# Optimization experiments

Hardware: AMD Instinct MI355X
Metric: run time of the kernel (lower is better)

## Reference

```python
import jax, jax.numpy as jnp
import numpy as np

B = 1
T_FRAMES = 512
LDIM = 512
D = 512
H = 8
DH = 64
L = 8
FF = 2048
CTX = 250
RATIOS = (8, 6, 5, 4)
MAX_PERIOD = 10000.0


def setup_inputs() -> dict:
    key = jax.random.key(0)
    ks = iter(jax.random.split(key, 80))
    def rn(shape, s=0.02):
        return jax.random.normal(next(ks), shape, jnp.float32) * s
    inp = {}
    inp['latent'] = rn((B, LDIM, T_FRAMES), 1.0)
    inp['emb_std'] = jax.random.uniform(next(ks), (LDIM,), jnp.float32, 0.5, 1.5)
    inp['emb_mean'] = rn((LDIM,), 0.1)
    inp['quant_w'] = rn((D, LDIM)); inp['quant_b'] = jnp.zeros((D,))
    inp['up_w'] = rn((D, D, 4)); inp['up_b'] = jnp.zeros((D,))
    inp['n1w'] = jnp.ones((L, D)); inp['n1b'] = jnp.zeros((L, D))
    inp['ipw'] = rn((L, 3 * D, D)); inp['ipb'] = jnp.zeros((L, 3 * D))
    inp['opw'] = rn((L, D, D)); inp['opb'] = jnp.zeros((L, D))
    inp['ls1'] = jnp.full((L, D), 0.01)
    inp['n2w'] = jnp.ones((L, D)); inp['n2b'] = jnp.zeros((L, D))
    inp['l1w'] = rn((L, FF, D)); inp['l1b'] = jnp.zeros((L, FF))
    inp['l2w'] = rn((L, D, FF)); inp['l2b'] = jnp.zeros((L, D))
    inp['ls2'] = jnp.full((L, D), 0.01)
    inp['tproj_w'] = rn((D, D)); inp['tproj_b'] = jnp.zeros((D,))
    inp['dc0_w'] = rn((1024, D, 7)); inp['dc0_b'] = jnp.zeros((1024,))
    ch = 1024
    for i, r in enumerate(RATIOS, 1):
        co = ch // 2
        inp['t%d_w' % i] = rn((ch, co, 2 * r)); inp['t%d_b' % i] = jnp.zeros((co,))
        inp['r%da_w' % i] = rn((co // 2, co, 3)); inp['r%da_b' % i] = jnp.zeros((co // 2,))
        inp['r%db_w' % i] = rn((co, co // 2, 1)); inp['r%db_b' % i] = jnp.zeros((co,))
        ch = co
    inp['df_w'] = rn((1, 64, 7)); inp['df_b'] = jnp.zeros((1,))
    return {k: jnp.asarray(v, jnp.float32) for k, v in inp.items()}


def _ln(x, w, b):
    m = x.mean(-1, keepdims=True)
    v = ((x - m) ** 2).mean(-1, keepdims=True)
    return (x - m) / jnp.sqrt(v + 1e-5) * w + b


def _rope(x, cos, sin):
    # x: (B,T,H,DH); cos/sin: (T,1,DH//2)
    b_, t_, h_, d_ = x.shape
    xr = x.reshape(b_, t_, h_, d_ // 2, 2)
    re, im = xr[..., 0], xr[..., 1]
    out = jnp.stack([re * cos - im * sin, re * sin + im * cos], axis=-1)
    return out.reshape(b_, t_, h_, d_)


def _conv(x, w, b, stride=1):
    # StreamingConv1d non-streaming: left-pad by k-stride (zeros), then valid conv.
    k = w.shape[-1]
    pad = k - stride
    if pad > 0:
        x = jnp.pad(x, ((0, 0), (0, 0), (pad, 0)))
    y = jax.lax.conv_general_dilated(x, w, (stride,), 'VALID',
                                     dimension_numbers=('NCH', 'OIH', 'NCH'))
    return y + b[None, :, None]


def _convtr(x, w, b, stride):
    # torch ConvTranspose1d, padding=0: w is (in, out, k); L_out=(L-1)*stride+k
    k = w.shape[-1]
    w2 = jnp.swapaxes(jnp.flip(w, -1), 0, 1)  # (out, in, k)
    y = jax.lax.conv_general_dilated(x, w2, (1,), [(k - 1, k - 1)],
                                     lhs_dilation=(stride,),
                                     dimension_numbers=('NCH', 'OIH', 'NCH'))
    return y + b[None, :, None]


def _forward(latent, emb_std, emb_mean, quant_w, quant_b, up_w, up_b,
             n1w, n1b, ipw, ipb, opw, opb, ls1, n2w, n2b, l1w, l1b, l2w, l2b, ls2,
             tproj_w, tproj_b, dc0_w, dc0_b,
             t1_w, t1_b, r1a_w, r1a_b, r1b_w, r1b_b,
             t2_w, t2_b, r2a_w, r2a_b, r2b_w, r2b_b,
             t3_w, t3_b, r3a_w, r3a_b, r3b_w, r3b_b,
             t4_w, t4_b, r4a_w, r4a_b, r4b_w, r4b_b,
             df_w, df_b):
    # denormalize + quantizer output proj (1x1 conv)
    x = latent * emb_std[None, :, None] + emb_mean[None, :, None]
    x = jnp.einsum('od,bdt->bot', quant_w, x) + quant_b[None, :, None]
    # upsample (raw convtr, no trimming)
    x = _convtr(x, up_w, up_b, 2)
    z = jnp.swapaxes(x, 1, 2)  # (B, T, D)
    T = z.shape[1]
    # windowed causal additive mask: attend to previous `CTX` positions incl. self
    pos = jnp.arange(T)
    delta = pos[:, None] - pos[None, :]
    mask = jnp.where((delta >= 0) & (delta < CTX), 0.0, -jnp.inf).astype(jnp.float32)
    # RoPE tables (offset = 0)
    fr = jnp.exp(jnp.arange(DH // 2, dtype=jnp.float32) * (-np.log(MAX_PERIOD) * 2.0 / DH))
    ang = jnp.arange(T, dtype=jnp.float32)[:, None, None] * fr  # (T,1,DH//2)
    cos, sin = jnp.cos(ang), jnp.sin(ang)
    scale = 1.0 / np.sqrt(DH)

    def step(h, p):
        n1w_, n1b_, ipw_, ipb_, opw_, opb_, ls1_, n2w_, n2b_, l1w_, l1b_, l2w_, l2b_, ls2_ = p
        hn = _ln(h, n1w_, n1b_)
        qkv = (jnp.einsum('btd,ed->bte', hn, ipw_) + ipb_).reshape(B, T, 3, H, DH)
        q, k, v = qkv[:, :, 0], qkv[:, :, 1], qkv[:, :, 2]
        q = _rope(q, cos, sin)
        k = _rope(k, cos, sin)
        s = jnp.einsum('bqhd,bkhd->bhqk', q, k) * scale + mask
        a = jax.nn.softmax(s, axis=-1)
        o = jnp.einsum('bhqk,bkhd->bqhd', a, v).reshape(B, T, D)
        o = jnp.einsum('btd,ed->bte', o, opw_) + opb_
        h = h + ls1_ * o
        hn2 = _ln(h, n2w_, n2b_)
        ff = jax.nn.gelu(jnp.einsum('btd,fd->btf', hn2, l1w_) + l1b_, approximate=False)
        ff = jnp.einsum('btf,df->btd', ff, l2w_) + l2b_
        h = h + ls2_ * ff
        return h, None

    z, _ = jax.lax.scan(step, z, (n1w, n1b, ipw, ipb, opw, opb, ls1,
                                  n2w, n2b, l1w, l1b, l2w, l2b, ls2))
    z = jnp.einsum('btd,ed->bte', z, tproj_w) + tproj_b
    z = jnp.swapaxes(z, 1, 2)  # (B, D, T)
    # SEANet decoder
    z = _conv(z, dc0_w, dc0_b, 1)
    stages = ((t1_w, t1_b, r1a_w, r1a_b, r1b_w, r1b_b, 8),
              (t2_w, t2_b, r2a_w, r2a_b, r2b_w, r2b_b, 6),
              (t3_w, t3_b, r3a_w, r3a_b, r3b_w, r3b_b, 5),
              (t4_w, t4_b, r4a_w, r4a_b, r4b_w, r4b_b, 4))
    for tw, tb, raw_, rab_, rbw_, rbb_, st in stages:
        z = jax.nn.elu(z)
        z = _convtr(z, tw, tb, st)
        v2 = _conv(jax.nn.elu(z), raw_, rab_, 1)
        v2 = _conv(jax.nn.elu(v2), rbw_, rbb_, 1)
        z = z + v2  # residual block skip
    z = jax.nn.elu(z)
    z = _conv(z, df_w, df_b, 1)
    return z  # (B, 1, T_samples)


def reference(latent, emb_std, emb_mean, quant_w, quant_b, up_w, up_b,
              n1w, n1b, ipw, ipb, opw, opb, ls1, n2w, n2b, l1w, l1b, l2w, l2b, ls2,
              tproj_w, tproj_b, dc0_w, dc0_b,
              t1_w, t1_b, r1a_w, r1a_b, r1b_w, r1b_b,
              t2_w, t2_b, r2a_w, r2a_b, r2b_w, r2b_b,
              t3_w, t3_b, r3a_w, r3a_b, r3b_w, r3b_b,
              t4_w, t4_b, r4a_w, r4a_b, r4b_w, r4b_b,
              df_w, df_b):
    return _forward(latent, emb_std, emb_mean, quant_w, quant_b, up_w, up_b,
                    n1w, n1b, ipw, ipb, opw, opb, ls1, n2w, n2b, l1w, l1b, l2w, l2b, ls2,
                    tproj_w, tproj_b, dc0_w, dc0_b,
                    t1_w, t1_b, r1a_w, r1a_b, r1b_w, r1b_b,
                    t2_w, t2_b, r2a_w, r2a_b, r2b_w, r2b_b,
                    t3_w, t3_b, r3a_w, r3a_b, r3b_w, r3b_b,
                    t4_w, t4_b, r4a_w, r4a_b, r4b_w, r4b_b,
                    df_w, df_b)
```

## Files before the change

kernel.cpp:

```cpp
#include <hip/hip_runtime.h>
#include <math.h>

typedef __attribute__((ext_vector_type(8))) short short8;
typedef __attribute__((ext_vector_type(4))) float f32x4;

#define MFMA16(a, b, c) __builtin_amdgcn_mfma_f32_16x16x32_bf16((a), (b), (c), 0, 0, 0)

__device__ __forceinline__ unsigned bfu(float f) {
    unsigned u = __float_as_uint(f);
    return (u + 0x7fffu + ((u >> 16) & 1u)) >> 16;
}

__device__ __forceinline__ void swz_block(unsigned& bx, unsigned& by, unsigned& bz) {
    unsigned gx = gridDim.x, gy = gridDim.y, gz = gridDim.z;
    unsigned nb = gx * gy * gz;
    unsigned d = blockIdx.x + gx * (blockIdx.y + gy * blockIdx.z);
    if ((nb & 7u) == 0u) d = (d & 7u) * (nb >> 3) + (d >> 3);
    bx = d % gx;
    unsigned r = d / gx;
    by = r % gy;
    bz = r / gy;
}

static constexpr int TT   = 1026;
static constexpr int T_S1 = 8216;
static constexpr int T_S2 = 49302;
static constexpr int T_S3 = 246515;
static constexpr int T_S4 = 986064;

static constexpr int NCH    = 8;
static constexpr int LC     = T_S4 / NCH;
static constexpr int LE_MAX = LC + 8;

static constexpr size_t O_X0  = 0;
static constexpr size_t O_XQ  = 262144;
static constexpr size_t O_XU  = 524288;
static constexpr size_t O_Z   = 1049600;
static constexpr size_t O_HN  = 1574912;
static constexpr size_t O_QKV = 2100224;
static constexpr size_t O_AO  = 3676160;
static constexpr size_t O_FF  = 4201472;
static constexpr size_t O_COS = 6302720;
static constexpr size_t O_SIN = 6335552;
static constexpr size_t O_ZT  = 6368384;
static constexpr size_t O_ZC  = 6893696;
static constexpr size_t O_D0  = 7419008;
static constexpr size_t O_Z1  = 8469632;
static constexpr size_t O_V1  = 12676224;
static constexpr size_t O_PS1 = 16000000;
static constexpr size_t O_Z2  = 31553920;
static constexpr size_t O_V2  = 0;
static constexpr size_t O_Z3  = 0;
static constexpr size_t O_V3  = 31553920;
static constexpr size_t O_Z4C = 31553920;
static constexpr size_t O_VAC = 39442944;

static inline int cdiv(int a, int b) { return (a + b - 1) / b; }

__global__ __launch_bounds__(256) void addp_k(float* __restrict__ y,
    const float* __restrict__ p, unsigned long long pstr, int np, int n4)
{
    int i = blockIdx.x * 256 + threadIdx.x;
    if (i >= n4) return;
    float4 s = ((float4*)y)[i];
    for (int z = 0; z < np; z++) {
        float4 q = ((const float4*)(p + (size_t)z * pstr))[i];
        s.x += q.x; s.y += q.y; s.z += q.z; s.w += q.w;
    }
    ((float4*)y)[i] = s;
}

__global__ __launch_bounds__(256) void embed_k(const float* __restrict__ lat,
    const float* __restrict__ sd, const float* __restrict__ mn, float* __restrict__ y)
{
    int i = blockIdx.x * 256 + threadIdx.x;
    if (i >= 512 * 512) return;
    int c = i >> 9;
    y[i] = lat[i] * sd[c] + mn[c];
}

__global__ __launch_bounds__(256) void rope_tables(float* __restrict__ cs, float* __restrict__ sn)
{
    int idx = blockIdx.x * 256 + threadIdx.x;
    if (idx >= TT * 32) return;
    int i = idx & 31;
    int t = idx >> 5;
    float fr = expf(-(float)i * (logf(10000.f) / 32.f));
    float ang = (float)t * fr;
    cs[idx] = cosf(ang);
    sn[idx] = sinf(ang);
}

__global__ __launch_bounds__(256) void rope_apply(float* __restrict__ qkv,
    const float* __restrict__ cs, const float* __restrict__ sn)
{
    int idx = blockIdx.x * 256 + threadIdx.x;
    if (idx >= TT * 8 * 32) return;
    int i = idx & 31;
    int h = (idx >> 5) & 7;
    int t = idx >> 8;
    float c = cs[t * 32 + i], s = sn[t * 32 + i];
    size_t base = (size_t)t * 1536 + h * 64 + 2 * i;
    float re = qkv[base], im = qkv[base + 1];
    qkv[base]     = re * c - im * s;
    qkv[base + 1] = re * s + im * c;
    base += 512;
    re = qkv[base]; im = qkv[base + 1];
    qkv[base]     = re * c - im * s;
    qkv[base + 1] = re * s + im * c;
}

__global__ __launch_bounds__(256) void transpose_k(const float* __restrict__ in,
    float* __restrict__ out, int R, int C)
{
    __shared__ float tile[32][33];
    int c0 = blockIdx.x * 32, r0 = blockIdx.y * 32;
    int tx = threadIdx.x & 31, ty = threadIdx.x >> 5;
    for (int dy = ty; dy < 32; dy += 8) {
        int r = r0 + dy, c = c0 + tx;
        tile[dy][tx] = (r < R && c < C) ? in[(size_t)r * C + c] : 0.f;
    }
    __syncthreads();
    for (int dy = ty; dy < 32; dy += 8) {
        int c = c0 + dy, r = r0 + tx;
        if (c < C && r < R) out[(size_t)c * R + r] = tile[tx][dy];
    }
}

__global__ __launch_bounds__(256) void ln_kernel(const float* __restrict__ x,
    const float* __restrict__ w, const float* __restrict__ b, float* __restrict__ y)
{
    int t = blockIdx.x, tid = threadIdx.x;
    const float* xr = x + (size_t)t * 512;
    float v0 = xr[tid], v1 = xr[tid + 256];
    float s = v0 + v1, q = v0 * v0 + v1 * v1;
    for (int off = 32; off; off >>= 1) {
        s += __shfl_down(s, off);
        q += __shfl_down(q, off);
    }
    __shared__ float ss[4], qq[4], mb[2];
    int wid = tid >> 6, lane = tid & 63;
    if (lane == 0) { ss[wid] = s; qq[wid] = q; }
    __syncthreads();
    if (tid == 0) {
        float S = ss[0] + ss[1] + ss[2] + ss[3];
        float Q = qq[0] + qq[1] + qq[2] + qq[3];
        float m = S * (1.f / 512.f);
        float var = Q * (1.f / 512.f) - m * m;
        mb[0] = m;
        mb[1] = rsqrtf(var + 1e-5f);
    }
    __syncthreads();
    float m = mb[0], inv = mb[1];
    y[(size_t)t * 512 + tid]       = (v0 - m) * inv * w[tid] + b[tid];
    y[(size_t)t * 512 + tid + 256] = (v1 - m) * inv * w[tid + 256] + b[tid + 256];
}

__global__ __launch_bounds__(256) void attn_kernel(const float* __restrict__ qkv,
    float* __restrict__ o)
{
    int t = blockIdx.x, h = blockIdx.y, tid = threadIdx.x;
    __shared__ float sq[64];
    __shared__ float sp[256];
    __shared__ float red[256];
    __shared__ float pacc[4][64];
    int klo = t - 249; if (klo < 0) klo = 0;
    int kc = t - klo + 1;
    if (tid < 64) sq[tid] = qkv[(size_t)t * 1536 + h * 64 + tid];
    __syncthreads();
    float sval = -3.0e38f;
    if (tid < kc) {
        const float* kr = qkv + (size_t)(klo + tid) * 1536 + 512 + h * 64;
        float d = 0.f;
#pragma unroll 8
        for (int i = 0; i < 64; i++) d += sq[i] * kr[i];
        sval = d * 0.125f;
    }
    red[tid] = sval;
    __syncthreads();
    for (int s2 = 128; s2 > 0; s2 >>= 1) {
        if (tid < s2) red[tid] = fmaxf(red[tid], red[tid + s2]);
        __syncthreads();
    }
    float m = red[0];
    __syncthreads();
    float p = (tid < kc) ? __expf(sval - m) : 0.f;
    sp[tid] = p;
    red[tid] = p;
    __syncthreads();
    for (int s2 = 128; s2 > 0; s2 >>= 1) {
        if (tid < s2) red[tid] += red[tid + s2];
        __syncthreads();
    }
    float inv = 1.f / red[0];
    int d = tid & 63, g = tid >> 6;
    float a = 0.f;
#pragma unroll 4
    for (int kk = g; kk < kc; kk += 4)
        a += sp[kk] * qkv[(size_t)(klo + kk) * 1536 + 1024 + h * 64 + d];
    pacc[g][d] = a;
    __syncthreads();
    if (tid < 64) {
        float r = (pacc[0][tid] + pacc[1][tid] + pacc[2][tid] + pacc[3][tid]) * inv;
        o[(size_t)t * 512 + h * 64 + tid] = r;
    }
}

template <int EPI>
__global__ __launch_bounds__(256, 3) void mfma_gemm(const float* __restrict__ A,
    const float* __restrict__ Wt, const float* __restrict__ bias,
    const float* __restrict__ ls, float* __restrict__ C, int M, int N, int K)
{
    constexpr int STR = 72;
    __shared__ unsigned short sA[128 * STR];
    __shared__ unsigned short sB[128 * STR];
    int tid = threadIdx.x;
    unsigned bxs, bys, bzs; swz_block(bxs, bys, bzs);
    int m0 = bys * 128, n0 = bxs * 128;
    int w = tid >> 6, lane = tid & 63;
    int wm = (w >> 1) * 64, wn = (w & 1) * 64;
    int row15 = lane & 15, q8 = (lane >> 4) * 8;
    int rb = tid >> 3;
    int sg = (tid & 7) * 8;
    f32x4 acc[4][4] = {};
    float4 av[8], bv[8];
    const float4 z4 = make_float4(0.f, 0.f, 0.f, 0.f);

    auto prefetch = [&](int k0) {
#pragma unroll
        for (int it = 0; it < 4; it++) {
            int r = rb + it * 32;
            int gm = m0 + r;
            if (gm < M) {
                const float4* p = (const float4*)(A + (size_t)gm * K + k0 + sg);
                av[2 * it] = p[0]; av[2 * it + 1] = p[1];
            } else { av[2 * it] = z4; av[2 * it + 1] = z4; }
            int gn = n0 + r;
            if (gn < N) {
                const float4* p = (const float4*)(Wt + (size_t)gn * K + k0 + sg);
                bv[2 * it] = p[0]; bv[2 * it + 1] = p[1];
            } else { bv[2 * it] = z4; bv[2 * it + 1] = z4; }
        }
    };

    prefetch(0);
    for (int k0 = 0; k0 < K; k0 += 64) {
        __syncthreads();
#pragma unroll
        for (int it = 0; it < 4; it++) {
            int r = rb + it * 32;
            unsigned* d = (unsigned*)&sA[r * STR + sg];
            float4 f0 = av[2 * it], f1 = av[2 * it + 1];
            d[0] = bfu(f0.x) | (bfu(f0.y) << 16); d[1] = bfu(f0.z) | (bfu(f0.w) << 16);
            d[2] = bfu(f1.x) | (bfu(f1.y) << 16); d[3] = bfu(f1.z) | (bfu(f1.w) << 16);
            d = (unsigned*)&sB[r * STR + sg];
            f0 = bv[2 * it]; f1 = bv[2 * it + 1];
            d[0] = bfu(f0.x) | (bfu(f0.y) << 16); d[1] = bfu(f0.z) | (bfu(f0.w) << 16);
            d[2] = bfu(f1.x) | (bfu(f1.y) << 16); d[3] = bfu(f1.z) | (bfu(f1.w) << 16);
        }
        __syncthreads();
        if (k0 + 64 < K) prefetch(k0 + 64);
#pragma unroll
        for (int kk = 0; kk < 64; kk += 32) {
            short8 af[4], bf[4];
#pragma unroll
            for (int f = 0; f < 4; f++) {
                af[f] = *(const short8*)&sA[(wm + f * 16 + row15) * STR + kk + q8];
                bf[f] = *(const short8*)&sB[(wn + f * 16 + row15) * STR + kk + q8];
            }
#pragma unroll
            for (int i = 0; i < 4; i++)
#pragma unroll
                for (int j = 0; j < 4; j++)
                    acc[i][j] = MFMA16(af[i], bf[j], acc[i][j]);
        }
    }
    int rq = (lane >> 4) * 4;
#pragma unroll
    for (int i = 0; i < 4; i++) {
#pragma unroll
        for (int r = 0; r < 4; r++) {
            int m = m0 + wm + i * 16 + rq + r;
            if (m >= M) continue;
#pragma unroll
            for (int j = 0; j < 4; j++) {
                int n = n0 + wn + j * 16 + row15;
                float v = acc[i][j][r] + bias[n];
                size_t idx = (size_t)m * N + n;
                if (EPI == 0) C[idx] = v;
                else if (EPI == 1) C[idx] = 0.5f * v * (1.f + erff(v * 0.70710678118654752f));
                else C[idx] += ls[n] * v;
            }
        }
    }
}

template <int K, bool ELU_IN, bool ACC, bool PART>
__global__ __launch_bounds__(256, 2) void mfma_conv(
    const float* __restrict__ x, const float* __restrict__ w,
    const float* __restrict__ bias, float* __restrict__ y, float* __restrict__ part,
    unsigned long long pstr,
    int Ci, int Co, int x_str, int Tx, int x_t0, int Ty, int y_t0, int to_lo, int to_hi,
    int nz)
{
    constexpr int TL = 128 + K - 1;
    constexpr int SX = 40;
    constexpr int SW = 40;
    constexpr int NX = (32 * TL + 255) / 256;
    constexpr int NW4 = 2 * K;
    __shared__ unsigned short sX[TL * SX];
    __shared__ unsigned short sW[K * 64 * SW];
    int tid = threadIdx.x;
    unsigned bxs, bys, bzs; swz_block(bxs, bys, bzs);
    int co0 = bys * 64;
    int t_base = to_lo + bxs * 128;
    int zi = (int)bzs;
    int cpz = (Ci / 32) / nz;
    int ci_b = zi * cpz * 32, ci_e = ci_b + cpz * 32;
    int w_id = tid >> 6, lane = tid & 63;
    int wm = (w_id >> 1) * 32, wn = (w_id & 1) * 64;
    int row15 = lane & 15, q8 = (lane >> 4) * 8;
    f32x4 acc[2][4] = {};
    float xv[NX];
    float4 wv4[NW4];
    const float4 z4 = make_float4(0.f, 0.f, 0.f, 0.f);

    auto prefetch = [&](int ci0) {
#pragma unroll
        for (int it = 0; it < NX; it++) {
            int i = tid + it * 256;
            float v = 0.f;
            if (i < 32 * TL) {
                int ci = i / TL, tl = i - ci * TL;
                int gl = t_base - (K - 1) + tl - x_t0;
                if (gl >= 0 && gl < Tx) v = x[(size_t)(ci0 + ci) * x_str + gl];
            }
            xv[it] = v;
        }
#pragma unroll
        for (int it = 0; it < NW4; it++) {
            int i4 = tid + it * 256;
            int co = i4 / (8 * K), r4 = i4 - co * (8 * K);
            wv4[it] = (co0 + co < Co)
                ? *(const float4*)(w + ((size_t)(co0 + co) * Ci + ci0) * K + r4 * 4)
                : z4;
        }
    };
    auto commit = [&]() {
#pragma unroll
        for (int it = 0; it < NX; it++) {
            int i = tid + it * 256;
            if (i < 32 * TL) {
                int ci = i / TL, tl = i - ci * TL;
                float v = xv[it];
                if (ELU_IN) v = v > 0.f ? v : __expf(v) - 1.f;
                sX[tl * SX + ci] = (unsigned short)bfu(v);
            }
        }
#pragma unroll
        for (int it = 0; it < NW4; it++) {
            int i4 = tid + it * 256;
            int co = i4 / (8 * K), r4 = i4 - co * (8 * K);
            float4 f = wv4[it];
#pragma unroll
            for (int e = 0; e < 4; e++) {
                int k = r4 * 4 + e;
                int ci = k / K, j = k - ci * K;
                float fv = (e == 0) ? f.x : (e == 1) ? f.y : (e == 2) ? f.z : f.w;
                sW[(j * 64 + co) * SW + ci] = (unsigned short)bfu(fv);
            }
        }
    };

    prefetch(ci_b);
    for (int ci0 = ci_b; ci0 < ci_e; ci0 += 32) {
        __syncthreads();
        commit();
        __syncthreads();
        if (ci0 + 32 < ci_e) prefetch(ci0 + 32);
#pragma unroll
        for (int j = 0; j < K; j++) {
            short8 af[2], bf[4];
#pragma unroll
            for (int f = 0; f < 2; f++)
                af[f] = *(const short8*)&sW[(j * 64 + wm + f * 16 + row15) * SW + q8];
#pragma unroll
            for (int f = 0; f < 4; f++)
                bf[f] = *(const short8*)&sX[(wn + f * 16 + row15 + j) * SX + q8];
#pragma unroll
            for (int i = 0; i < 2; i++)
#pragma unroll
                for (int f = 0; f < 4; f++)
                    acc[i][f] = MFMA16(af[i], bf[f], acc[i][f]);
        }
    }
    int rq = (lane >> 4) * 4;
#pragma unroll
    for (int i = 0; i < 2; i++) {
#pragma unroll
        for (int r = 0; r < 4; r++) {
            int co = co0 + wm + i * 16 + rq + r;
            if (co >= Co) continue;
            float b = bias[co];
#pragma unroll
            for (int f = 0; f < 4; f++) {
                int t = t_base + wn + f * 16 + row15;
                if (t < to_hi) {
                    size_t idx = (size_t)co * Ty + (t - y_t0);
                    if (PART && zi > 0) {
                        part[(size_t)(zi - 1) * pstr + idx] = acc[i][f][r];
                    } else {
                        float v = acc[i][f][r] + b;
                        if (ACC) y[idx] += v; else y[idx] = v;
                    }
                }
            }
        }
    }
}

template <int S, int PG, bool ELU_IN>
__global__ __launch_bounds__(256, 3) void mfma_convtr(
    const float* __restrict__ x, const float* __restrict__ w,
    const float* __restrict__ bias, float* __restrict__ y,
    int Ci, int Co, int Ti, int Ty, int y_t0, int q_lo, int to_lo, int to_hi)
{
    constexpr int SX = 40;
    constexpr int SW = 40;
    constexpr int NW = PG * 2;
    __shared__ unsigned short sX[256 * SX];
    __shared__ unsigned short sW[PG * 16 * SW];
    int tid = threadIdx.x;
    unsigned bxs, bys, bzs; swz_block(bxs, bys, bzs);
    int co0 = bys * 16;
    int q0 = q_lo + (int)bxs * 256;
    int p0 = (int)bzs * PG;
    int w_id = tid >> 6, lane = tid & 63;
    int row15 = lane & 15, q8 = (lane >> 4) * 8;
    f32x4 acc[PG][4] = {};
    int q = q0 + tid;
    bool qok0 = (q >= 0) && (q < Ti);
    bool qok1 = (q >= 1) && (q <= Ti);
    float xv0[16], xv1[16], wv[NW];

    auto prefetch = [&](int ci0) {
#pragma unroll
        for (int it = 0; it < 16; it++) {
            const float* xr = x + (size_t)(ci0 + it) * Ti;
            xv0[it] = qok0 ? xr[q] : 0.f;
            xv1[it] = qok1 ? xr[q - 1] : 0.f;
        }
#pragma unroll
        for (int it = 0; it < NW; it++) {
            int i = tid + it * 256;
            int pl = i >> 9, r = i & 511;
            int co = r >> 5, k = r & 31;
            int ci = k >> 1, tap = k & 1;
            wv[it] = (p0 + pl < S)
                ? w[((size_t)(ci0 + ci) * Co + co0 + co) * (2 * S) + tap * S + p0 + pl]
                : 0.f;
        }
    };
    auto commit = [&]() {
#pragma unroll
        for (int it = 0; it < 16; it++) {
            float v0 = xv0[it], v1 = xv1[it];
            if (ELU_IN) {
                v0 = v0 > 0.f ? v0 : __expf(v0) - 1.f;
                v1 = v1 > 0.f ? v1 : __expf(v1) - 1.f;
            }
            *(unsigned*)&sX[tid * SX + 2 * it] = bfu(v0) | (bfu(v1) << 16);
        }
#pragma unroll
        for (int it = 0; it < NW; it++) {
            int i = tid + it * 256;
            int pl = i >> 9, r = i & 511;
            int co = r >> 5, k = r & 31;
            sW[(pl * 16 + co) * SW + k] = (unsigned short)bfu(wv[it]);
        }
    };

    prefetch(0);
    for (int ci0 = 0; ci0 < Ci; ci0 += 16) {
        __syncthreads();
        commit();
        __syncthreads();
        if (ci0 + 16 < Ci) prefetch(ci0 + 16);
        short8 bf[4];
#pragma unroll
        for (int f = 0; f < 4; f++)
            bf[f] = *(const short8*)&sX[(w_id * 64 + f * 16 + row15) * SX + q8];
#pragma unroll
        for (int p = 0; p < PG; p++) {
            short8 af = *(const short8*)&sW[(p * 16 + row15) * SW + q8];
#pragma unroll
            for (int f = 0; f < 4; f++)
                acc[p][f] = MFMA16(af, bf[f], acc[p][f]);
        }
    }
    int rq = (lane >> 4) * 4;
#pragma unroll
    for (int r = 0; r < 4; r++) {
        int co = co0 + rq + r;
        float b = bias[co];
#pragma unroll
        for (int f = 0; f < 4; f++) {
            int qq = q0 + w_id * 64 + f * 16 + row15;
#pragma unroll
            for (int p = 0; p < PG; p++) {
                int to = qq * S + p0 + p;
                if (p0 + p < S && to >= to_lo && to < to_hi)
                    y[(size_t)co * Ty + (to - y_t0)] = acc[p][f][r] + b;
            }
        }
    }
}

__global__ __launch_bounds__(256) void conv7_out_chunk(const float* __restrict__ z4c,
    const float* __restrict__ w, const float* __restrict__ bias,
    float* __restrict__ out, int ext0, int t0, int cnt)
{
    __shared__ float ws_w[64 * 7];
    int tl = blockIdx.x * 256 + threadIdx.x;
    for (int i = threadIdx.x; i < 448; i += 256) ws_w[i] = w[i];
    __syncthreads();
    if (tl >= cnt) return;
    int t = t0 + tl;
    float acc = bias[0];
    for (int ci = 0; ci < 64; ci++) {
        const float* xr = z4c + (size_t)ci * LE_MAX;
#pragma unroll
        for (int j = 0; j < 7; j++) {
            int tg = t - 6 + j;
            float v = 0.f;
            if (tg >= 0) {
                float z = xr[tg - ext0];
                v = z > 0.f ? z : __expf(z) - 1.f;
            }
            acc += ws_w[ci * 7 + j] * v;
        }
    }
    out[t] = acc;
}

template <int K, bool ELU_IN, bool ACC, bool PART>
static void conv_launch(const float* x, const float* w, const float* b, float* y,
    float* part, unsigned long long pstr,
    int Ci, int Co, int x_str, int Tx, int x_t0, int Ty, int y_t0, int to_lo, int to_hi,
    int nz, hipStream_t stream)
{
    dim3 g(cdiv(to_hi - to_lo, 128), cdiv(Co, 64), nz);
    mfma_conv<K, ELU_IN, ACC, PART><<<g, 256, 0, stream>>>(x, w, b, y, part, pstr,
        Ci, Co, x_str, Tx, x_t0, Ty, y_t0, to_lo, to_hi, nz);
}

template <int S, int PG, bool ELU_IN>
static void convtr_launch(const float* x, const float* w, const float* b, float* y,
    int Ci, int Co, int Ti, int Ty, int y_t0, int to_lo, int to_hi, hipStream_t stream)
{
    int q_lo = to_lo / S;
    int q_hi = (to_hi - 1) / S;
    dim3 g(cdiv(q_hi - q_lo + 1, 256), Co / 16, cdiv(S, PG));
    mfma_convtr<S, PG, ELU_IN><<<g, 256, 0, stream>>>(x, w, b, y, Ci, Co, Ti, Ty, y_t0, q_lo, to_lo, to_hi);
}

extern "C" void kernel_launch(void* const* d_in, const int* in_sizes, int n_in,
                              void* d_out, int out_size, void* d_ws, size_t ws_size,
                              hipStream_t stream)
{
    const float* latent  = (const float*)d_in[0];
    const float* emb_std = (const float*)d_in[1];
    const float* emb_mean= (const float*)d_in[2];
    const float* quant_w = (const float*)d_in[3];
    const float* quant_b = (const float*)d_in[4];
    const float* up_w    = (const float*)d_in[5];
    const float* up_b    = (const float*)d_in[6];
    const float* n1w     = (const float*)d_in[7];
    const float* n1b     = (const float*)d_in[8];
    const float* ipw     = (const float*)d_in[9];
    const float* ipb     = (const float*)d_in[10];
    const float* opw     = (const float*)d_in[11];
    const float* opb     = (const float*)d_in[12];
    const float* ls1     = (const float*)d_in[13];
    const float* n2w     = (const float*)d_in[14];
    const float* n2b     = (const float*)d_in[15];
    const float* l1w     = (const float*)d_in[16];
    const float* l1b     = (const float*)d_in[17];
    const float* l2w     = (const float*)d_in[18];
    const float* l2b     = (const float*)d_in[19];
    const float* ls2     = (const float*)d_in[20];
    const float* tproj_w = (const float*)d_in[21];
    const float* tproj_b = (const float*)d_in[22];
    const float* dc0_w   = (const float*)d_in[23];
    const float* dc0_b   = (const float*)d_in[24];
    const float* df_w    = (const float*)d_in[49];
    const float* df_b    = (const float*)d_in[50];

    float* W = (float*)d_ws;
    float* OUT = (float*)d_out;

    embed_k<<<cdiv(512 * 512, 256), 256, 0, stream>>>(latent, emb_std, emb_mean, W + O_X0);
    conv_launch<1, false, false, true>(W + O_X0, quant_w, quant_b, W + O_XQ,
        W + O_QKV, 262144ULL, 512, 512, 512, 512, 0, 512, 0, 0, 512, 4, stream);
    addp_k<<<cdiv(262144 / 4, 256), 256, 0, stream>>>(W + O_XQ, W + O_QKV, 262144ULL, 3, 262144 / 4);
    convtr_launch<2, 1, false>(W + O_XQ, up_w, up_b, W + O_XU,
        512, 512, 512, TT, 0, 0, TT, stream);
    transpose_k<<<dim3(cdiv(TT, 32), cdiv(512, 32)), 256, 0, stream>>>(W + O_XU, W + O_Z, 512, TT);
    rope_tables<<<cdiv(TT * 32, 256), 256, 0, stream>>>(W + O_COS, W + O_SIN);

    for (int l = 0; l < 8; l++) {
        ln_kernel<<<TT, 256, 0, stream>>>(W + O_Z, n1w + l * 512, n1b + l * 512, W + O_HN);
        mfma_gemm<0><<<dim3(1536 / 128, cdiv(TT, 128)), 256, 0, stream>>>(
            W + O_HN, ipw + (size_t)l * 1536 * 512, ipb + l * 1536, nullptr, W + O_QKV, TT, 1536, 512);
        rope_apply<<<cdiv(TT * 8 * 32, 256), 256, 0, stream>>>(W + O_QKV, W + O_COS, W + O_SIN);
        attn_kernel<<<dim3(TT, 8), 256, 0, stream>>>(W + O_QKV, W + O_AO);
        mfma_gemm<2><<<dim3(512 / 128, cdiv(TT, 128)), 256, 0, stream>>>(
            W + O_AO, opw + (size_t)l * 512 * 512, opb + l * 512, ls1 + l * 512, W + O_Z, TT, 512, 512);
        ln_kernel<<<TT, 256, 0, stream>>>(W + O_Z, n2w + l * 512, n2b + l * 512, W + O_HN);
        mfma_gemm<1><<<dim3(2048 / 128, cdiv(TT, 128)), 256, 0, stream>>>(
            W + O_HN, l1w + (size_t)l * 2048 * 512, l1b + l * 2048, nullptr, W + O_FF, TT, 2048, 512);
        mfma_gemm<2><<<dim3(512 / 128, cdiv(TT, 128)), 256, 0, stream>>>(
            W + O_FF, l2w + (size_t)l * 512 * 2048, l2b + l * 512, ls2 + l * 512, W + O_Z, TT, 512, 2048);
    }

    mfma_gemm<0><<<dim3(512 / 128, cdiv(TT, 128)), 256, 0, stream>>>(
        W + O_Z, tproj_w, tproj_b, nullptr, W + O_ZT, TT, 512, 512);
    transpose_k<<<dim3(cdiv(512, 32), cdiv(TT, 32)), 256, 0, stream>>>(W + O_ZT, W + O_ZC, TT, 512);
    conv_launch<7, false, false, true>(W + O_ZC, dc0_w, dc0_b, W + O_D0,
        W + O_FF, 1050624ULL, 512, 1024, TT, TT, 0, TT, 0, 0, TT, 2, stream);
    addp_k<<<cdiv(1050624 / 4, 256), 256, 0, stream>>>(W + O_D0, W + O_FF, 1050624ULL, 1, 1050624 / 4);

    {
        const float* tw = (const float*)d_in[25]; const float* tb = (const float*)d_in[26];
        const float* raw = (const float*)d_in[27]; const float* rab = (const float*)d_in[28];
        const float* rbw = (const float*)d_in[29]; const float* rbb = (const float*)d_in[30];
        convtr_launch<8, 2, true>(W + O_D0, tw, tb, W + O_Z1,
            1024, 512, TT, T_S1, 0, 0, T_S1, stream);
        conv_launch<3, true, false, true>(W + O_Z1, raw, rab, W + O_V1,
            W + O_PS1, 2103296ULL, 512, 256, T_S1, T_S1, 0, T_S1, 0, 0, T_S1, 2, stream);
        addp_k<<<cdiv(2103296 / 4, 256), 256, 0, stream>>>(W + O_V1, W + O_PS1, 2103296ULL, 1, 2103296 / 4);
        conv_launch<1, true, true, false>(W + O_V1, rbw, rbb, W + O_Z1,
            nullptr, 0ULL, 256, 512, T_S1, T_S1, 0, T_S1, 0, 0, T_S1, 1, stream);
    }
    {
        const float* tw = (const float*)d_in[31]; const float* tb = (const float*)d_in[32];
        const float* raw = (const float*)d_in[33]; const float* rab = (const float*)d_in[34];
        const float* rbw = (const float*)d_in[35]; const float* rbb = (const float*)d_in[36];
        convtr_launch<6, 2, true>(W + O_Z1, tw, tb, W + O_Z2,
            512, 256, T_S1, T_S2, 0, 0, T_S2, stream);
        conv_launch<3, true, false, false>(W + O_Z2, raw, rab, W + O_V2,
            nullptr, 0ULL, 256, 128, T_S2, T_S2, 0, T_S2, 0, 0, T_S2, 1, stream);
        conv_launch<1, true, true, false>(W + O_V2, rbw, rbb, W + O_Z2,
            nullptr, 0ULL, 128, 256, T_S2, T_S2, 0, T_S2, 0, 0, T_S2, 1, stream);
    }
    {
        const float* tw = (const float*)d_in[37]; const float* tb = (const float*)d_in[38];
        const float* raw = (const float*)d_in[39]; const float* rab = (const float*)d_in[40];
        const float* rbw = (const float*)d_in[41]; const float* rbb = (const float*)d_in[42];
        convtr_launch<5, 2, true>(W + O_Z2, tw, tb, W + O_Z3,
            256, 128, T_S2, T_S3, 0, 0, T_S3, stream);
        conv_launch<3, true, false, false>(W + O_Z3, raw, rab, W + O_V3,
            nullptr, 0ULL, 128, 64, T_S3, T_S3, 0, T_S3, 0, 0, T_S3, 1, stream);
        conv_launch<1, true, true, false>(W + O_V3, rbw, rbb, W + O_Z3,
            nullptr, 0ULL, 64, 128, T_S3, T_S3, 0, T_S3, 0, 0, T_S3, 1, stream);
    }
    {
        const float* tw = (const float*)d_in[43]; const float* tb = (const float*)d_in[44];
        const float* raw = (const float*)d_in[45]; const float* rab = (const float*)d_in[46];
        const float* rbw = (const float*)d_in[47]; const float* rbb = (const float*)d_in[48];
        for (int c = 0; c < NCH; c++) {
            int t0 = c * LC;
            int ext0 = (c == 0) ? 0 : t0 - 8;
            int Le = t0 + LC - ext0;
            int vlo = (c == 0) ? 0 : ext0 + 2;
            convtr_launch<4, 2, true>(W + O_Z3, tw, tb, W + O_Z4C,
                128, 64, T_S3, LE_MAX, ext0, ext0, ext0 + Le, stream);
            conv_launch<3, true, false, false>(W + O_Z4C, raw, rab, W + O_VAC,
                nullptr, 0ULL, 64, 32, LE_MAX, Le, ext0, LE_MAX, ext0, vlo, ext0 + Le, 1, stream);
            conv_launch<1, true, true, false>(W + O_VAC, rbw, rbb, W + O_Z4C,
                nullptr, 0ULL, 32, 64, LE_MAX, Le, ext0, LE_MAX, ext0, vlo, ext0 + Le, 1, stream);
            conv7_out_chunk<<<dim3(cdiv(LC, 256), 1), 256, 0, stream>>>(
                W + O_Z4C, df_w, df_b, OUT, ext0, t0, LC);
        }
    }
}
```

Measured before the change: 6.720 ms.

## Recast transposed convolutions as polyphase K=2 convolutions through the MFMA conv kernel

```diff
diff --git a/kernel.cpp b/kernel.cpp
--- a/kernel.cpp
+++ b/kernel.cpp
@@ -54,6 +54,8 @@
 static constexpr size_t O_V3  = 31553920;
 static constexpr size_t O_Z4C = 31553920;
 static constexpr size_t O_VAC = 39442944;
+static constexpr size_t O_WS4 = 43388928;
+static constexpr size_t O_WS3 = 44176256;
 
 static inline int cdiv(int a, int b) { return (a + b - 1) / b; }
 
@@ -68,6 +70,17 @@
         s.x += q.x; s.y += q.y; s.z += q.z; s.w += q.w;
     }
     ((float4*)y)[i] = s;
+}
+
+__global__ __launch_bounds__(256) void wreorder_tr(const float* __restrict__ w,
+    float* __restrict__ wp, int Ci, int Co, int S, int n)
+{
+    int i = blockIdx.x * 256 + threadIdx.x;
+    if (i >= n) return;
+    int o = i / (Ci * 2), r = i - o * (Ci * 2);
+    int ci = r >> 1, j = r & 1;
+    int co = o / S, p = o - co * S;
+    wp[i] = w[((size_t)ci * Co + co) * (2 * S) + (1 - j) * S + p];
 }
 
 __global__ __launch_bounds__(256) void embed_k(const float* __restrict__ lat,
@@ -295,21 +308,23 @@
     }
 }
 
-template <int K, bool ELU_IN, bool ACC, bool PART>
+template <int K, int SHF, bool ELU_IN, bool ACC, bool PART>
 __global__ __launch_bounds__(256, 2) void mfma_conv(
     const float* __restrict__ x, const float* __restrict__ w,
     const float* __restrict__ bias, float* __restrict__ y, float* __restrict__ part,
     unsigned long long pstr,
     int Ci, int Co, int x_str, int Tx, int x_t0, int Ty, int y_t0, int to_lo, int to_hi,
-    int nz)
+    int sh_lo, int sh_hi, int nz)
 {
     constexpr int TL = 128 + K - 1;
     constexpr int SX = 40;
     constexpr int SW = 40;
     constexpr int NX = (32 * TL + 255) / 256;
     constexpr int NW4 = 2 * K;
+    constexpr int LTS = (SHF > 0) ? 64 * 130 : 1;
     __shared__ unsigned short sX[TL * SX];
     __shared__ unsigned short sW[K * 64 * SW];
+    __shared__ float ldsT[LTS];
     int tid = threadIdx.x;
     unsigned bxs, bys, bzs; swz_block(bxs, bys, bzs);
     int co0 = bys * 64;
@@ -395,122 +410,55 @@
         }
     }
     int rq = (lane >> 4) * 4;
-#pragma unroll
-    for (int i = 0; i < 2; i++) {
-#pragma unroll
-        for (int r = 0; r < 4; r++) {
-            int co = co0 + wm + i * 16 + rq + r;
-            if (co >= Co) continue;
-            float b = bias[co];
-#pragma unroll
-            for (int f = 0; f < 4; f++) {
-                int t = t_base + wn + f * 16 + row15;
-                if (t < to_hi) {
-                    size_t idx = (size_t)co * Ty + (t - y_t0);
-                    if (PART && zi > 0) {
-                        part[(size_t)(zi - 1) * pstr + idx] = acc[i][f][r];
-                    } else {
-                        float v = acc[i][f][r] + b;
-                        if (ACC) y[idx] += v; else y[idx] = v;
+    if constexpr (SHF > 0) {
+        __syncthreads();
+#pragma unroll
+        for (int i = 0; i < 2; i++) {
+#pragma unroll
+            for (int r = 0; r < 4; r++) {
+                int ol = wm + i * 16 + rq + r;
+                float b = bias[(co0 + ol) / SHF];
+#pragma unroll
+                for (int f = 0; f < 4; f++) {
+                    int tl = wn + f * 16 + row15;
+                    ldsT[ol * 130 + tl] = acc[i][f][r] + b;
+                }
+            }
+        }
+        __syncthreads();
+        int co_lo = co0 / SHF;
+        int cnt = (co0 + 63) / SHF - co_lo + 1;
+        int tot = cnt * 128 * SHF;
+        for (int e = tid; e < tot; e += 256) {
+            int cr = e / (128 * SHF), u = e - cr * (128 * SHF);
+            int t_rel = u / SHF, p = u - t_rel * SHF;
+            int co = co_lo + cr;
+            int o = co * SHF + p - co0;
+            int to = (t_base + t_rel) * SHF + p;
+            if (o >= 0 && o < 64 && to >= sh_lo && to < sh_hi)
+                y[(size_t)co * Ty + (to - y_t0)] = ldsT[o * 130 + t_rel];
+        }
+    } else {
+#pragma unroll
+        for (int i = 0; i < 2; i++) {
+#pragma unroll
+            for (int r = 0; r < 4; r++) {
+                int co = co0 + wm + i * 16 + rq + r;
+                if (co >= Co) continue;
+                float b = bias[co];
+#pragma unroll
+                for (int f = 0; f < 4; f++) {
+                    int t = t_base + wn + f * 16 + row15;
+                    if (t < to_hi) {
+                        size_t idx = (size_t)co * Ty + (t - y_t0);
+                        if (PART && zi > 0) {
+                            part[(size_t)(zi - 1) * pstr + idx] = acc[i][f][r];
+                        } else {
+                            float v = acc[i][f][r] + b;
+                            if (ACC) y[idx] += v; else y[idx] = v;
+                        }
                     }
                 }
-            }
-        }
-    }
-}
-
-template <int S, int PG, bool ELU_IN>
-__global__ __launch_bounds__(256, 3) void mfma_convtr(
-    const float* __restrict__ x, const float* __restrict__ w,
-    const float* __restrict__ bias, float* __restrict__ y,
-    int Ci, int Co, int Ti, int Ty, int y_t0, int q_lo, int to_lo, int to_hi)
-{
-    constexpr int SX = 40;
-    constexpr int SW = 40;
-    constexpr int NW = PG * 2;
-    __shared__ unsigned short sX[256 * SX];
-    __shared__ unsigned short sW[PG * 16 * SW];
-    int tid = threadIdx.x;
-    unsigned bxs, bys, bzs; swz_block(bxs, bys, bzs);
-    int co0 = bys * 16;
-    int q0 = q_lo + (int)bxs * 256;
-    int p0 = (int)bzs * PG;
-    int w_id = tid >> 6, lane = tid & 63;
-    int row15 = lane & 15, q8 = (lane >> 4) * 8;
-    f32x4 acc[PG][4] = {};
-    int q = q0 + tid;
-    bool qok0 = (q >= 0) && (q < Ti);
-    bool qok1 = (q >= 1) && (q <= Ti);
-    float xv0[16], xv1[16], wv[NW];
-
-    auto prefetch = [&](int ci0) {
-#pragma unroll
-        for (int it = 0; it < 16; it++) {
-            const float* xr = x + (size_t)(ci0 + it) * Ti;
-            xv0[it] = qok0 ? xr[q] : 0.f;
-            xv1[it] = qok1 ? xr[q - 1] : 0.f;
-        }
-#pragma unroll
-        for (int it = 0; it < NW; it++) {
-            int i = tid + it * 256;
-            int pl = i >> 9, r = i & 511;
-            int co = r >> 5, k = r & 31;
-            int ci = k >> 1, tap = k & 1;
-            wv[it] = (p0 + pl < S)
-                ? w[((size_t)(ci0 + ci) * Co + co0 + co) * (2 * S) + tap * S + p0 + pl]
-                : 0.f;
-        }
-    };
-    auto commit = [&]() {
-#pragma unroll
-        for (int it = 0; it < 16; it++) {
-            float v0 = xv0[it], v1 = xv1[it];
-            if (ELU_IN) {
-                v0 = v0 > 0.f ? v0 : __expf(v0) - 1.f;
-                v1 = v1 > 0.f ? v1 : __expf(v1) - 1.f;
-            }
-            *(unsigned*)&sX[tid * SX + 2 * it] = bfu(v0) | (bfu(v1) << 16);
-        }
-#pragma unroll
-        for (int it = 0; it < NW; it++) {
-            int i = tid + it * 256;
-            int pl = i >> 9, r = i & 511;
-            int co = r >> 5, k = r & 31;
-            sW[(pl * 16 + co) * SW + k] = (unsigned short)bfu(wv[it]);
-        }
-    };
-
-    prefetch(0);
-    for (int ci0 = 0; ci0 < Ci; ci0 += 16) {
-        __syncthreads();
-        commit();
-        __syncthreads();
-        if (ci0 + 16 < Ci) prefetch(ci0 + 16);
-        short8 bf[4];
-#pragma unroll
-        for (int f = 0; f < 4; f++)
-            bf[f] = *(const short8*)&sX[(w_id * 64 + f * 16 + row15) * SX + q8];
-#pragma unroll
-        for (int p = 0; p < PG; p++) {
-            short8 af = *(const short8*)&sW[(p * 16 + row15) * SW + q8];
-#pragma unroll
-            for (int f = 0; f < 4; f++)
-                acc[p][f] = MFMA16(af, bf[f], acc[p][f]);
-        }
-    }
-    int rq = (lane >> 4) * 4;
-#pragma unroll
-    for (int r = 0; r < 4; r++) {
-        int co = co0 + rq + r;
-        float b = bias[co];
-#pragma unroll
-        for (int f = 0; f < 4; f++) {
-            int qq = q0 + w_id * 64 + f * 16 + row15;
-#pragma unroll
-            for (int p = 0; p < PG; p++) {
-                int to = qq * S + p0 + p;
-                if (p0 + p < S && to >= to_lo && to < to_hi)
-                    y[(size_t)co * Ty + (to - y_t0)] = acc[p][f][r] + b;
             }
         }
     }
@@ -550,18 +498,19 @@
     int nz, hipStream_t stream)
 {
     dim3 g(cdiv(to_hi - to_lo, 128), cdiv(Co, 64), nz);
-    mfma_conv<K, ELU_IN, ACC, PART><<<g, 256, 0, stream>>>(x, w, b, y, part, pstr,
-        Ci, Co, x_str, Tx, x_t0, Ty, y_t0, to_lo, to_hi, nz);
-}
-
-template <int S, int PG, bool ELU_IN>
-static void convtr_launch(const float* x, const float* w, const float* b, float* y,
+    mfma_conv<K, 0, ELU_IN, ACC, PART><<<g, 256, 0, stream>>>(x, w, b, y, part, pstr,
+        Ci, Co, x_str, Tx, x_t0, Ty, y_t0, to_lo, to_hi, 0, 0, nz);
+}
+
+template <int S, bool ELU_IN>
+static void convtr2_launch(const float* x, const float* wp, const float* b, float* y,
     int Ci, int Co, int Ti, int Ty, int y_t0, int to_lo, int to_hi, hipStream_t stream)
 {
     int q_lo = to_lo / S;
-    int q_hi = (to_hi - 1) / S;
-    dim3 g(cdiv(q_hi - q_lo + 1, 256), Co / 16, cdiv(S, PG));
-    mfma_convtr<S, PG, ELU_IN><<<g, 256, 0, stream>>>(x, w, b, y, Ci, Co, Ti, Ty, y_t0, q_lo, to_lo, to_hi);
+    int q_hi = cdiv(to_hi, S);
+    dim3 g(cdiv(q_hi - q_lo, 128), (Co * S) / 64, 1);
+    mfma_conv<2, S, ELU_IN, false, false><<<g, 256, 0, stream>>>(x, wp, b, y, nullptr, 0,
+        Ci, Co * S, Ti, Ti, 0, Ty, y_t0, q_lo, q_hi, to_lo, to_hi, 1);
 }
 
 extern "C" void kernel_launch(void* const* d_in, const int* in_sizes, int n_in,
@@ -603,7 +552,8 @@
     conv_launch<1, false, false, true>(W + O_X0, quant_w, quant_b, W + O_XQ,
         W + O_QKV, 262144ULL, 512, 512, 512, 512, 0, 512, 0, 0, 512, 4, stream);
     addp_k<<<cdiv(262144 / 4, 256), 256, 0, stream>>>(W + O_XQ, W + O_QKV, 262144ULL, 3, 262144 / 4);
-    convtr_launch<2, 1, false>(W + O_XQ, up_w, up_b, W + O_XU,
+    wreorder_tr<<<cdiv(1048576, 256), 256, 0, stream>>>(up_w, W + O_QKV, 512, 512, 2, 1048576);
+    convtr2_launch<2, false>(W + O_XQ, W + O_QKV, up_b, W + O_XU,
         512, 512, 512, TT, 0, 0, TT, stream);
     transpose_k<<<dim3(cdiv(TT, 32), cdiv(512, 32)), 256, 0, stream>>>(W + O_XU, W + O_Z, 512, TT);
     rope_tables<<<cdiv(TT * 32, 256), 256, 0, stream>>>(W + O_COS, W + O_SIN);
@@ -634,7 +584,8 @@
         const float* tw = (const float*)d_in[25]; const float* tb = (const float*)d_in[26];
         const float* raw = (const float*)d_in[27]; const float* rab = (const float*)d_in[28];
         const float* rbw = (const float*)d_in[29]; const float* rbb = (const float*)d_in[30];
-        convtr_launch<8, 2, true>(W + O_D0, tw, tb, W + O_Z1,
+        wreorder_tr<<<cdiv(8388608, 256), 256, 0, stream>>>(tw, W + O_PS1, 1024, 512, 8, 8388608);
+        convtr2_launch<8, true>(W + O_D0, W + O_PS1, tb, W + O_Z1,
             1024, 512, TT, T_S1, 0, 0, T_S1, stream);
         conv_launch<3, true, false, true>(W + O_Z1, raw, rab, W + O_V1,
             W + O_PS1, 2103296ULL, 512, 256, T_S1, T_S1, 0, T_S1, 0, 0, T_S1, 2, stream);
@@ -646,7 +597,8 @@
         const float* tw = (const float*)d_in[31]; const float* tb = (const float*)d_in[32];
         const float* raw = (const float*)d_in[33]; const float* rab = (const float*)d_in[34];
         const float* rbw = (const float*)d_in[35]; const float* rbb = (const float*)d_in[36];
-        convtr_launch<6, 2, true>(W + O_Z1, tw, tb, W + O_Z2,
+        wreorder_tr<<<cdiv(1572864, 256), 256, 0, stream>>>(tw, W + O_PS1, 512, 256, 6, 1572864);
+        convtr2_launch<6, true>(W + O_Z1, W + O_PS1, tb, W + O_Z2,
             512, 256, T_S1, T_S2, 0, 0, T_S2, stream);
         conv_launch<3, true, false, false>(W + O_Z2, raw, rab, W + O_V2,
             nullptr, 0ULL, 256, 128, T_S2, T_S2, 0, T_S2, 0, 0, T_S2, 1, stream);
@@ -657,7 +609,8 @@
         const float* tw = (const float*)d_in[37]; const float* tb = (const float*)d_in[38];
         const float* raw = (const float*)d_in[39]; const float* rab = (const float*)d_in[40];
         const float* rbw = (const float*)d_in[41]; const float* rbb = (const float*)d_in[42];
-        convtr_launch<5, 2, true>(W + O_Z2, tw, tb, W + O_Z3,
+        wreorder_tr<<<cdiv(327680, 256), 256, 0, stream>>>(tw, W + O_WS3, 256, 128, 5, 327680);
+        convtr2_launch<5, true>(W + O_Z2, W + O_WS3, tb, W + O_Z3,
             256, 128, T_S2, T_S3, 0, 0, T_S3, stream);
         conv_launch<3, true, false, false>(W + O_Z3, raw, rab, W + O_V3,
             nullptr, 0ULL, 128, 64, T_S3, T_S3, 0, T_S3, 0, 0, T_S3, 1, stream);
@@ -668,12 +621,13 @@
         const float* tw = (const float*)d_in[43]; const float* tb = (const float*)d_in[44];
         const float* raw = (const float*)d_in[45]; const float* rab = (const float*)d_in[46];
         const float* rbw = (const float*)d_in[47]; const float* rbb = (const float*)d_in[48];
+        wreorder_tr<<<cdiv(65536, 256), 256, 0, stream>>>(tw, W + O_WS4, 128, 64, 4, 65536);
         for (int c = 0; c < NCH; c++) {
             int t0 = c * LC;
             int ext0 = (c == 0) ? 0 : t0 - 8;
             int Le = t0 + LC - ext0;
             int vlo = (c == 0) ? 0 : ext0 + 2;
-            convtr_launch<4, 2, true>(W + O_Z3, tw, tb, W + O_Z4C,
+            convtr2_launch<4, true>(W + O_Z3, W + O_WS4, tb, W + O_Z4C,
                 128, 64, T_S3, LE_MAX, ext0, ext0, ext0 + Le, stream);
             conv_launch<3, true, false, false>(W + O_Z4C, raw, rab, W + O_VAC,
                 nullptr, 0ULL, 64, 32, LE_MAX, Le, ext0, LE_MAX, ext0, vlo, ext0 + Le, 1, stream);
```

Measured after the change: 6.560 ms. 1.02x faster.
